# Kernel optimization log

Hardware: AMD Instinct MI355X
Metric: run time of the kernel (lower is better)

The kernel has to match this reference:

```python
import jax, jax.numpy as jnp
import numpy as np
from jax import lax

NUM_KEYPOINTS = 17
OUT_CHANNELS = 18
IN_CHANNELS = 480
H, W = 256, 256
MAX_PROPOSALS = 30
KPT_THRE = 0.01
CENTER_POOL_K = 3
# map_size = (H + W)/2 = 256; 200 < 256 <= 300 -> 5x5 max pool branch (static)
NMS_POOL_K = 5


def _avg_pool_same(x, k):
    # torch F.avg_pool2d(k, stride=1, pad=(k-1)//2), count_include_pad=True
    s = lax.reduce_window(x, 0.0, lax.add, (1, k, k), (1, 1, 1), 'SAME')
    return s / float(k * k)


def _max_pool_same(x, k):
    return lax.reduce_window(x, -jnp.inf, lax.max, (1, k, k), (1, 1, 1), 'SAME')


def setup_inputs() -> dict:
    key = jax.random.key(0)
    k1, k2 = jax.random.split(key)
    features = jax.random.normal(k1, (1, IN_CHANNELS, H, W), dtype=jnp.float32)
    conv_w = jax.random.normal(k2, (OUT_CHANNELS, IN_CHANNELS), dtype=jnp.float32) * 0.001
    # bias = -log((1-p)/p), p = 0.01
    conv_b = jnp.full((OUT_CHANNELS,), -np.log((1 - 0.01) / 0.01), dtype=jnp.float32)
    return {"features": features, "conv_w": conv_w, "conv_b": conv_b}


def reference(features, conv_w, conv_b):
    # 1x1 conv == channel contraction
    hm = jnp.einsum('bchw,oc->bohw', features, conv_w) + conv_b[None, :, None, None]
    hm = jnp.clip(jax.nn.sigmoid(hm), 1e-4, 1.0 - 1e-4)  # _sigmoid

    center = hm[:, -1, :, :]                 # [1, H, W] (no flip test)
    pool = _avg_pool_same(center, CENTER_POOL_K)
    center = (center + pool) * 0.5

    maxm = _max_pool_same(center, NMS_POOL_K)
    center = center * (maxm == center).astype(center.dtype)

    scores, pos_ind = lax.top_k(center.reshape(-1), MAX_PROPOSALS)
    x = pos_ind % W
    y = pos_ind // W
    instance_coord = jnp.stack((y, x), axis=1)            # [K, 2]
    # _sample_feats: features[0][:, y, x] -> [K, C]
    instance_param = features[0, :, y, x].T
    valid = scores > KPT_THRE                              # padded-select mask
    return instance_coord, scores, instance_param, valid
```

## Files before the change

### kernel.cpp

```cpp
#include <hip/hip_runtime.h>
#include <cfloat>
#include <cmath>

#define IC 480
#define OC 18
#define HH 256
#define WW 256
#define HW_ 65536
#define NPROP 30
#define CG 8
#define CPG 60
#define CAP 6144


__global__ __launch_bounds__(256) void k_dot(const float* __restrict__ f,
                                             const float* __restrict__ w,
                                             float* __restrict__ partial,
                                             int* __restrict__ counter) {
    __shared__ float sw[CPG];
    const int tid = threadIdx.x;
    const int cg = blockIdx.y;
    const int c0 = cg * CPG;
    if (tid < CPG) sw[tid] = w[17 * IC + c0 + tid];
    if (blockIdx.x == 0 && cg == 0 && tid == 0) *counter = 0;
    __syncthreads();
    const int p4 = blockIdx.x * 256 + tid;
    const float4* __restrict__ f4 = (const float4*)f;
    float ax = 0.f, ay = 0.f, az = 0.f, aw = 0.f;
    #pragma unroll 10
    for (int c = 0; c < CPG; ++c) {
        float4 v = f4[(size_t)(c0 + c) * (HW_ / 4) + p4];
        float wc = sw[c];
        ax = fmaf(v.x, wc, ax);
        ay = fmaf(v.y, wc, ay);
        az = fmaf(v.z, wc, az);
        aw = fmaf(v.w, wc, aw);
    }
    float4 r; r.x = ax; r.y = ay; r.z = az; r.w = aw;
    ((float4*)partial)[(size_t)cg * (HW_ / 4) + p4] = r;
}

__global__ __launch_bounds__(256) void k_pool(const float* __restrict__ partial,
                                              const float* __restrict__ conv_b,
                                              float* __restrict__ cand_val,
                                              int* __restrict__ cand_idx,
                                              int* __restrict__ counter) {
    const int TX = 32, TY = 8;
    __shared__ float sc[TY + 6][TX + 6];
    __shared__ float s2[TY + 4][TX + 4];
    const int tid = threadIdx.x;
    const int ox = blockIdx.x * TX, oy = blockIdx.y * TY;
    const float b = conv_b[OC - 1];

    for (int i = tid; i < (TY + 6) * (TX + 6); i += 256) {
        int ly = i / (TX + 6), lx = i % (TX + 6);
        int gy = oy - 3 + ly, gx = ox - 3 + lx;
        float v = 0.f;
        if (gy >= 0 && gy < HH && gx >= 0 && gx < WW) {
            int p = gy * WW + gx;
            float raw = b;
            #pragma unroll
            for (int g = 0; g < CG; ++g) raw += partial[g * HW_ + p];
            float s = 1.f / (1.f + expf(-raw));
            v = fminf(fmaxf(s, 1e-4f), 1.f - 1e-4f);
        }
        sc[ly][lx] = v;
    }
    __syncthreads();

    for (int i = tid; i < (TY + 4) * (TX + 4); i += 256) {
        int ly = i / (TX + 4), lx = i % (TX + 4);
        int gy = oy - 2 + ly, gx = ox - 2 + lx;
        float v = -FLT_MAX;
        if (gy >= 0 && gy < HH && gx >= 0 && gx < WW) {
            float sum = 0.f;
            #pragma unroll
            for (int dy = 0; dy < 3; ++dy)
                #pragma unroll
                for (int dx = 0; dx < 3; ++dx)
                    sum += sc[ly + dy][lx + dx];
            v = (sc[ly + 1][lx + 1] + sum / 9.0f) * 0.5f;
        }
        s2[ly][lx] = v;
    }
    __syncthreads();

    const int tx = tid & 31, ty = tid >> 5;
    float c = s2[ty + 2][tx + 2];
    float m = -FLT_MAX;
    #pragma unroll
    for (int dy = 0; dy < 5; ++dy)
        #pragma unroll
        for (int dx = 0; dx < 5; ++dx)
            m = fmaxf(m, s2[ty + dy][tx + dx]);
    if (m == c) {
        int slot = atomicAdd(counter, 1);
        if (slot < CAP) {
            cand_val[slot] = c;
            cand_idx[slot] = (oy + ty) * WW + (ox + tx);
        }
    }
}

__device__ __forceinline__ unsigned long long bsort64(unsigned long long key,
                                                      int lane) {
    #pragma unroll
    for (int k = 2; k <= 64; k <<= 1) {
        #pragma unroll
        for (int j = k >> 1; j > 0; j >>= 1) {
            unsigned long long o = __shfl_xor(key, j);
            bool lower = (lane & j) == 0;
            bool asc   = (lane & k) == 0;
            unsigned long long mn = key < o ? key : o;
            unsigned long long mx = key < o ? o : key;
            key = (lower == asc) ? mn : mx;
        }
    }
    return key;
}

__device__ __forceinline__ unsigned long long bmerge64(unsigned long long key,
                                                       int lane) {
    #pragma unroll
    for (int j = 32; j > 0; j >>= 1) {
        unsigned long long o = __shfl_xor(key, j);
        bool lower = (lane & j) == 0;
        unsigned long long mn = key < o ? key : o;
        unsigned long long mx = key < o ? o : key;
        key = lower ? mn : mx;
    }
    return key;
}

__global__ __launch_bounds__(512) void k_select(const float* __restrict__ cand_val,
                                                const int* __restrict__ cand_idx,
                                                const int* __restrict__ counter,
                                                float* __restrict__ out,
                                                int* __restrict__ selpix) {
    __shared__ unsigned long long lk[512];
    const int tid = threadIdx.x;
    const int lane = tid & 63, wv = tid >> 6;
    int n = *counter; if (n > CAP) n = CAP;

    unsigned long long R = 0;
    for (int base = wv * 64; base < n; base += 512) {
        int j = base + lane;
        unsigned long long key = 0;
        if (j < n) {
            unsigned fb = __float_as_uint(cand_val[j]);
            key = ((unsigned long long)fb << 32)
                | (unsigned long long)(0xFFFFFFFFu - (unsigned)cand_idx[j]);
        }
        key = bsort64(key, lane);
        unsigned long long crev = __shfl_xor(key, 63);
        R = R > crev ? R : crev;
        R = bmerge64(R, lane);
    }
    lk[tid] = R;
    __syncthreads();

    if (wv == 0) {
        R = lk[lane];
        #pragma unroll
        for (int w = 1; w < 8; ++w) {
            unsigned long long c = lk[w * 64 + lane];
            unsigned long long crev = __shfl_xor(c, 63);
            R = R > crev ? R : crev;
            R = bmerge64(R, lane);
        }
        int r = 63 - lane;
        if (r < NPROP) {
            float s = 0.f; int p = 0;
            if (R != 0) {
                s = __uint_as_float((unsigned)(R >> 32));
                p = (int)(0xFFFFFFFFu - (unsigned)(R & 0xFFFFFFFFu));
            }
            out[2 * r]     = (float)(p >> 8);
            out[2 * r + 1] = (float)(p & 255);
            out[60 + r] = s;
            out[60 + NPROP + NPROP * IC + r] = (s > 0.01f) ? 1.f : 0.f;
            selpix[r] = p;
        }
    }
}

__global__ __launch_bounds__(256) void k_gather(const float* __restrict__ f,
                                                const int* __restrict__ selpix,
                                                float* __restrict__ out) {
    __shared__ int sp[NPROP];
    const int tid = threadIdx.x;
    if (tid < NPROP) sp[tid] = selpix[tid];
    __syncthreads();
    int idx = blockIdx.x * 256 + tid;
    if (idx < IC * NPROP) {
        int c = idx / NPROP, i = idx % NPROP;
        out[60 + NPROP + idx] = f[(size_t)c * HW_ + sp[i]];
    }
}

extern "C" void kernel_launch(void* const* d_in, const int* in_sizes, int n_in,
                              void* d_out, int out_size, void* d_ws, size_t ws_size,
                              hipStream_t stream) {
    const float* features = (const float*)d_in[0];
    const float* conv_w   = (const float*)d_in[1];
    const float* conv_b   = (const float*)d_in[2];
    float* out = (float*)d_out;
    char* ws = (char*)d_ws;

    float* partial  = (float*)ws;
    float* cand_val = (float*)(ws + (2 << 20));
    int*   cand_idx = (int*)  (ws + (2 << 20) + CAP * 4);
    int*   counter  = (int*)  (ws + (2 << 20) + CAP * 8);
    int*   selpix   = (int*)  (ws + (2 << 20) + CAP * 8 + 16);

    k_dot   <<<dim3(HW_ / 1024, CG), 256, 0, stream>>>(features, conv_w,
                                                       partial, counter);
    k_pool  <<<dim3(WW / 32, HH / 8), 256, 0, stream>>>(partial, conv_b,
                                                        cand_val, cand_idx, counter);
    k_select<<<1, 512, 0, stream>>>(cand_val, cand_idx, counter, out, selpix);
    k_gather<<<(IC * NPROP + 255) / 256, 256, 0, stream>>>(features, selpix, out);
}
```

Before: 54.82 us.

## Fuse four kernels into one cooperative kernel with grid-wide syncs

Replaces the four separate launches (partial dot, pool/NMS, top-k select, gather) with a single cooperative kernel of 512 blocks that separates the stages with grid.sync(). The aim is to remove the launch overhead and inter-kernel gaps that dominate a short pipeline. The select stage now runs in one 256-thread block (4 waves instead of 8), so that serial phase does more work per wave. Each grid barrier adds its own cost, and a cooperative launch requires every block to be resident at once.

```diff
diff --git a/kernel.cpp b/kernel.cpp
--- a/kernel.cpp
+++ b/kernel.cpp
@@ -1,6 +1,9 @@
 #include <hip/hip_runtime.h>
+#include <hip/hip_cooperative_groups.h>
 #include <cfloat>
 #include <cmath>
+
+namespace cg = cooperative_groups;
 
 #define IC 480
 #define OC 18
@@ -8,99 +11,10 @@
 #define WW 256
 #define HW_ 65536
 #define NPROP 30
-#define CG 8
+#define NCG 8
 #define CPG 60
 #define CAP 6144
 
-
-__global__ __launch_bounds__(256) void k_dot(const float* __restrict__ f,
-                                             const float* __restrict__ w,
-                                             float* __restrict__ partial,
-                                             int* __restrict__ counter) {
-    __shared__ float sw[CPG];
-    const int tid = threadIdx.x;
-    const int cg = blockIdx.y;
-    const int c0 = cg * CPG;
-    if (tid < CPG) sw[tid] = w[17 * IC + c0 + tid];
-    if (blockIdx.x == 0 && cg == 0 && tid == 0) *counter = 0;
-    __syncthreads();
-    const int p4 = blockIdx.x * 256 + tid;
-    const float4* __restrict__ f4 = (const float4*)f;
-    float ax = 0.f, ay = 0.f, az = 0.f, aw = 0.f;
-    #pragma unroll 10
-    for (int c = 0; c < CPG; ++c) {
-        float4 v = f4[(size_t)(c0 + c) * (HW_ / 4) + p4];
-        float wc = sw[c];
-        ax = fmaf(v.x, wc, ax);
-        ay = fmaf(v.y, wc, ay);
-        az = fmaf(v.z, wc, az);
-        aw = fmaf(v.w, wc, aw);
-    }
-    float4 r; r.x = ax; r.y = ay; r.z = az; r.w = aw;
-    ((float4*)partial)[(size_t)cg * (HW_ / 4) + p4] = r;
-}
-
-__global__ __launch_bounds__(256) void k_pool(const float* __restrict__ partial,
-                                              const float* __restrict__ conv_b,
-                                              float* __restrict__ cand_val,
-                                              int* __restrict__ cand_idx,
-                                              int* __restrict__ counter) {
-    const int TX = 32, TY = 8;
-    __shared__ float sc[TY + 6][TX + 6];
-    __shared__ float s2[TY + 4][TX + 4];
-    const int tid = threadIdx.x;
-    const int ox = blockIdx.x * TX, oy = blockIdx.y * TY;
-    const float b = conv_b[OC - 1];
-
-    for (int i = tid; i < (TY + 6) * (TX + 6); i += 256) {
-        int ly = i / (TX + 6), lx = i % (TX + 6);
-        int gy = oy - 3 + ly, gx = ox - 3 + lx;
-        float v = 0.f;
-        if (gy >= 0 && gy < HH && gx >= 0 && gx < WW) {
-            int p = gy * WW + gx;
-            float raw = b;
-            #pragma unroll
-            for (int g = 0; g < CG; ++g) raw += partial[g * HW_ + p];
-            float s = 1.f / (1.f + expf(-raw));
-            v = fminf(fmaxf(s, 1e-4f), 1.f - 1e-4f);
-        }
-        sc[ly][lx] = v;
-    }
-    __syncthreads();
-
-    for (int i = tid; i < (TY + 4) * (TX + 4); i += 256) {
-        int ly = i / (TX + 4), lx = i % (TX + 4);
-        int gy = oy - 2 + ly, gx = ox - 2 + lx;
-        float v = -FLT_MAX;
-        if (gy >= 0 && gy < HH && gx >= 0 && gx < WW) {
-            float sum = 0.f;
-            #pragma unroll
-            for (int dy = 0; dy < 3; ++dy)
-                #pragma unroll
-                for (int dx = 0; dx < 3; ++dx)
-                    sum += sc[ly + dy][lx + dx];
-            v = (sc[ly + 1][lx + 1] + sum / 9.0f) * 0.5f;
-        }
-        s2[ly][lx] = v;
-    }
-    __syncthreads();
-
-    const int tx = tid & 31, ty = tid >> 5;
-    float c = s2[ty + 2][tx + 2];
-    float m = -FLT_MAX;
-    #pragma unroll
-    for (int dy = 0; dy < 5; ++dy)
-        #pragma unroll
-        for (int dx = 0; dx < 5; ++dx)
-            m = fmaxf(m, s2[ty + dy][tx + dx]);
-    if (m == c) {
-        int slot = atomicAdd(counter, 1);
-        if (slot < CAP) {
-            cand_val[slot] = c;
-            cand_idx[slot] = (oy + ty) * WW + (ox + tx);
-        }
-    }
-}
 
 __device__ __forceinline__ unsigned long long bsort64(unsigned long long key,
                                                       int lane) {
@@ -132,69 +46,152 @@
     return key;
 }
 
-__global__ __launch_bounds__(512) void k_select(const float* __restrict__ cand_val,
-                                                const int* __restrict__ cand_idx,
-                                                const int* __restrict__ counter,
-                                                float* __restrict__ out,
-                                                int* __restrict__ selpix) {
-    __shared__ unsigned long long lk[512];
+__global__ __launch_bounds__(256) void k_fused(const float* __restrict__ f,
+                                               const float* __restrict__ w,
+                                               const float* __restrict__ conv_b,
+                                               float* __restrict__ out,
+                                               float* __restrict__ partial,
+                                               float* __restrict__ cand_val,
+                                               int* __restrict__ cand_idx,
+                                               int* __restrict__ counter,
+                                               int* __restrict__ selpix) {
+    cg::grid_group grid = cg::this_grid();
     const int tid = threadIdx.x;
-    const int lane = tid & 63, wv = tid >> 6;
-    int n = *counter; if (n > CAP) n = CAP;
-
-    unsigned long long R = 0;
-    for (int base = wv * 64; base < n; base += 512) {
-        int j = base + lane;
-        unsigned long long key = 0;
-        if (j < n) {
-            unsigned fb = __float_as_uint(cand_val[j]);
-            key = ((unsigned long long)fb << 32)
-                | (unsigned long long)(0xFFFFFFFFu - (unsigned)cand_idx[j]);
-        }
-        key = bsort64(key, lane);
-        unsigned long long crev = __shfl_xor(key, 63);
-        R = R > crev ? R : crev;
-        R = bmerge64(R, lane);
-    }
-    lk[tid] = R;
-    __syncthreads();
-
-    if (wv == 0) {
-        R = lk[lane];
+    const int bid = blockIdx.x;
+
+    __shared__ float sw[CPG];
+    __shared__ float sc[14][38];
+    __shared__ float s2[12][36];
+    __shared__ unsigned long long lk[256];
+
+    {
+        const int cgi = bid >> 6;
+        const int bx  = bid & 63;
+        const int c0  = cgi * CPG;
+        if (tid < CPG) sw[tid] = w[17 * IC + c0 + tid];
+        if (bid == 0 && tid == 0) atomicExch(counter, 0);
+        __syncthreads();
+        const int p4 = bx * 256 + tid;
+        const float4* __restrict__ f4 = (const float4*)f;
+        float ax = 0.f, ay = 0.f, az = 0.f, aww = 0.f;
+        #pragma unroll 10
+        for (int c = 0; c < CPG; ++c) {
+            float4 v = f4[(size_t)(c0 + c) * (HW_ / 4) + p4];
+            float wc = sw[c];
+            ax  = fmaf(v.x, wc, ax);
+            ay  = fmaf(v.y, wc, ay);
+            az  = fmaf(v.z, wc, az);
+            aww = fmaf(v.w, wc, aww);
+        }
+        float4 r; r.x = ax; r.y = ay; r.z = az; r.w = aww;
+        ((float4*)partial)[(size_t)cgi * (HW_ / 4) + p4] = r;
+    }
+    grid.sync();
+
+    if (bid < 256) {
+        const int ox = (bid & 7) * 32, oy = (bid >> 3) * 8;
+        const float b = conv_b[OC - 1];
+        for (int i = tid; i < 14 * 38; i += 256) {
+            int ly = i / 38, lx = i % 38;
+            int gy = oy - 3 + ly, gx = ox - 3 + lx;
+            float v = 0.f;
+            if (gy >= 0 && gy < HH && gx >= 0 && gx < WW) {
+                int p = gy * WW + gx;
+                float raw = b;
+                #pragma unroll
+                for (int g = 0; g < NCG; ++g) raw += partial[g * HW_ + p];
+                float s = 1.f / (1.f + expf(-raw));
+                v = fminf(fmaxf(s, 1e-4f), 1.f - 1e-4f);
+            }
+            sc[ly][lx] = v;
+        }
+        __syncthreads();
+        for (int i = tid; i < 12 * 36; i += 256) {
+            int ly = i / 36, lx = i % 36;
+            int gy = oy - 2 + ly, gx = ox - 2 + lx;
+            float v = -FLT_MAX;
+            if (gy >= 0 && gy < HH && gx >= 0 && gx < WW) {
+                float sum = 0.f;
+                #pragma unroll
+                for (int dy = 0; dy < 3; ++dy)
+                    #pragma unroll
+                    for (int dx = 0; dx < 3; ++dx)
+                        sum += sc[ly + dy][lx + dx];
+                v = (sc[ly + 1][lx + 1] + sum / 9.0f) * 0.5f;
+            }
+            s2[ly][lx] = v;
+        }
+        __syncthreads();
+        const int tx = tid & 31, ty = tid >> 5;
+        float c = s2[ty + 2][tx + 2];
+        float m = -FLT_MAX;
         #pragma unroll
-        for (int w = 1; w < 8; ++w) {
-            unsigned long long c = lk[w * 64 + lane];
-            unsigned long long crev = __shfl_xor(c, 63);
+        for (int dy = 0; dy < 5; ++dy)
+            #pragma unroll
+            for (int dx = 0; dx < 5; ++dx)
+                m = fmaxf(m, s2[ty + dy][tx + dx]);
+        if (m == c) {
+            int slot = atomicAdd(counter, 1);
+            if (slot < CAP) {
+                cand_val[slot] = c;
+                cand_idx[slot] = (oy + ty) * WW + (ox + tx);
+            }
+        }
+    }
+    grid.sync();
+
+    if (bid == 0) {
+        const int lane = tid & 63, wv = tid >> 6;
+        int n = atomicAdd(counter, 0);
+        if (n > CAP) n = CAP;
+        unsigned long long R = 0;
+        for (int base = wv * 64; base < n; base += 256) {
+            int j = base + lane;
+            unsigned long long key = 0;
+            if (j < n) {
+                unsigned fb = __float_as_uint(cand_val[j]);
+                key = ((unsigned long long)fb << 32)
+                    | (unsigned long long)(0xFFFFFFFFu - (unsigned)cand_idx[j]);
+            }
+            key = bsort64(key, lane);
+            unsigned long long crev = __shfl_xor(key, 63);
             R = R > crev ? R : crev;
             R = bmerge64(R, lane);
         }
-        int r = 63 - lane;
-        if (r < NPROP) {
-            float s = 0.f; int p = 0;
-            if (R != 0) {
-                s = __uint_as_float((unsigned)(R >> 32));
-                p = (int)(0xFFFFFFFFu - (unsigned)(R & 0xFFFFFFFFu));
-            }
-            out[2 * r]     = (float)(p >> 8);
-            out[2 * r + 1] = (float)(p & 255);
-            out[60 + r] = s;
-            out[60 + NPROP + NPROP * IC + r] = (s > 0.01f) ? 1.f : 0.f;
-            selpix[r] = p;
-        }
-    }
-}
-
-__global__ __launch_bounds__(256) void k_gather(const float* __restrict__ f,
-                                                const int* __restrict__ selpix,
-                                                float* __restrict__ out) {
-    __shared__ int sp[NPROP];
-    const int tid = threadIdx.x;
-    if (tid < NPROP) sp[tid] = selpix[tid];
-    __syncthreads();
-    int idx = blockIdx.x * 256 + tid;
-    if (idx < IC * NPROP) {
-        int c = idx / NPROP, i = idx % NPROP;
-        out[60 + NPROP + idx] = f[(size_t)c * HW_ + sp[i]];
+        lk[tid] = R;
+        __syncthreads();
+        if (wv == 0) {
+            R = lk[lane];
+            #pragma unroll
+            for (int ww = 1; ww < 4; ++ww) {
+                unsigned long long c2 = lk[ww * 64 + lane];
+                unsigned long long crev = __shfl_xor(c2, 63);
+                R = R > crev ? R : crev;
+                R = bmerge64(R, lane);
+            }
+            int r = 63 - lane;
+            if (r < NPROP) {
+                float s = 0.f; int p = 0;
+                if (R != 0) {
+                    s = __uint_as_float((unsigned)(R >> 32));
+                    p = (int)(0xFFFFFFFFu - (unsigned)(R & 0xFFFFFFFFu));
+                }
+                out[2 * r]     = (float)(p >> 8);
+                out[2 * r + 1] = (float)(p & 255);
+                out[60 + r] = s;
+                out[60 + NPROP + NPROP * IC + r] = (s > 0.01f) ? 1.f : 0.f;
+                selpix[r] = p;
+            }
+        }
+    }
+    grid.sync();
+
+    {
+        int idx = bid * 256 + tid;
+        if (idx < IC * NPROP) {
+            int c = idx / NPROP, i = idx % NPROP;
+            out[60 + NPROP + idx] = f[(size_t)c * HW_ + selpix[i]];
+        }
     }
 }
 
@@ -213,10 +210,11 @@
     int*   counter  = (int*)  (ws + (2 << 20) + CAP * 8);
     int*   selpix   = (int*)  (ws + (2 << 20) + CAP * 8 + 16);
 
-    k_dot   <<<dim3(HW_ / 1024, CG), 256, 0, stream>>>(features, conv_w,
-                                                       partial, counter);
-    k_pool  <<<dim3(WW / 32, HH / 8), 256, 0, stream>>>(partial, conv_b,
-                                                        cand_val, cand_idx, counter);
-    k_select<<<1, 512, 0, stream>>>(cand_val, cand_idx, counter, out, selpix);
-    k_gather<<<(IC * NPROP + 255) / 256, 256, 0, stream>>>(features, selpix, out);
-}
+    void* args[9] = {
+        (void*)&features, (void*)&conv_w, (void*)&conv_b, (void*)&out,
+        (void*)&partial, (void*)&cand_val, (void*)&cand_idx,
+        (void*)&counter, (void*)&selpix
+    };
+    hipLaunchCooperativeKernel((const void*)k_fused, dim3(512), dim3(256),
+                               args, 0, stream);
+}
```

New measurement: 206.9 us. +277.5%, slower.

## Fuse pooling/NMS and top-k selection via last-block-done pattern

Applied to the files above, without the earlier changes.

Merges the pooling/NMS kernel and the single-block selection kernel into one launch. Each block increments a global done counter after emitting candidates, and the last block to finish performs the bitonic top-k over all candidates with 256 threads instead of 512. This removes one kernel launch and its inter-kernel gap, at the cost of a serialized tail in one block with fewer threads and extra atomics.

```diff
diff --git a/kernel.cpp b/kernel.cpp
--- a/kernel.cpp
+++ b/kernel.cpp
@@ -8,7 +8,7 @@
 #define WW 256
 #define HW_ 65536
 #define NPROP 30
-#define CG 8
+#define NCG 8
 #define CPG 60
 #define CAP 6144
 
@@ -16,13 +16,14 @@
 __global__ __launch_bounds__(256) void k_dot(const float* __restrict__ f,
                                              const float* __restrict__ w,
                                              float* __restrict__ partial,
-                                             int* __restrict__ counter) {
+                                             int* __restrict__ counter,
+                                             int* __restrict__ done) {
     __shared__ float sw[CPG];
     const int tid = threadIdx.x;
     const int cg = blockIdx.y;
     const int c0 = cg * CPG;
     if (tid < CPG) sw[tid] = w[17 * IC + c0 + tid];
-    if (blockIdx.x == 0 && cg == 0 && tid == 0) *counter = 0;
+    if (blockIdx.x == 0 && cg == 0 && tid == 0) { *counter = 0; *done = 0; }
     __syncthreads();
     const int p4 = blockIdx.x * 256 + tid;
     const float4* __restrict__ f4 = (const float4*)f;
@@ -38,68 +39,6 @@
     }
     float4 r; r.x = ax; r.y = ay; r.z = az; r.w = aw;
     ((float4*)partial)[(size_t)cg * (HW_ / 4) + p4] = r;
-}
-
-__global__ __launch_bounds__(256) void k_pool(const float* __restrict__ partial,
-                                              const float* __restrict__ conv_b,
-                                              float* __restrict__ cand_val,
-                                              int* __restrict__ cand_idx,
-                                              int* __restrict__ counter) {
-    const int TX = 32, TY = 8;
-    __shared__ float sc[TY + 6][TX + 6];
-    __shared__ float s2[TY + 4][TX + 4];
-    const int tid = threadIdx.x;
-    const int ox = blockIdx.x * TX, oy = blockIdx.y * TY;
-    const float b = conv_b[OC - 1];
-
-    for (int i = tid; i < (TY + 6) * (TX + 6); i += 256) {
-        int ly = i / (TX + 6), lx = i % (TX + 6);
-        int gy = oy - 3 + ly, gx = ox - 3 + lx;
-        float v = 0.f;
-        if (gy >= 0 && gy < HH && gx >= 0 && gx < WW) {
-            int p = gy * WW + gx;
-            float raw = b;
-            #pragma unroll
-            for (int g = 0; g < CG; ++g) raw += partial[g * HW_ + p];
-            float s = 1.f / (1.f + expf(-raw));
-            v = fminf(fmaxf(s, 1e-4f), 1.f - 1e-4f);
-        }
-        sc[ly][lx] = v;
-    }
-    __syncthreads();
-
-    for (int i = tid; i < (TY + 4) * (TX + 4); i += 256) {
-        int ly = i / (TX + 4), lx = i % (TX + 4);
-        int gy = oy - 2 + ly, gx = ox - 2 + lx;
-        float v = -FLT_MAX;
-        if (gy >= 0 && gy < HH && gx >= 0 && gx < WW) {
-            float sum = 0.f;
-            #pragma unroll
-            for (int dy = 0; dy < 3; ++dy)
-                #pragma unroll
-                for (int dx = 0; dx < 3; ++dx)
-                    sum += sc[ly + dy][lx + dx];
-            v = (sc[ly + 1][lx + 1] + sum / 9.0f) * 0.5f;
-        }
-        s2[ly][lx] = v;
-    }
-    __syncthreads();
-
-    const int tx = tid & 31, ty = tid >> 5;
-    float c = s2[ty + 2][tx + 2];
-    float m = -FLT_MAX;
-    #pragma unroll
-    for (int dy = 0; dy < 5; ++dy)
-        #pragma unroll
-        for (int dx = 0; dx < 5; ++dx)
-            m = fmaxf(m, s2[ty + dy][tx + dx]);
-    if (m == c) {
-        int slot = atomicAdd(counter, 1);
-        if (slot < CAP) {
-            cand_val[slot] = c;
-            cand_idx[slot] = (oy + ty) * WW + (ox + tx);
-        }
-    }
 }
 
 __device__ __forceinline__ unsigned long long bsort64(unsigned long long key,
@@ -132,24 +71,97 @@
     return key;
 }
 
-__global__ __launch_bounds__(512) void k_select(const float* __restrict__ cand_val,
-                                                const int* __restrict__ cand_idx,
-                                                const int* __restrict__ counter,
-                                                float* __restrict__ out,
-                                                int* __restrict__ selpix) {
-    __shared__ unsigned long long lk[512];
+__global__ __launch_bounds__(256) void k_pool_select(
+        const float* __restrict__ partial, const float* __restrict__ conv_b,
+        float* __restrict__ cand_val, int* __restrict__ cand_idx,
+        int* __restrict__ counter, int* __restrict__ done,
+        float* __restrict__ out, int* __restrict__ selpix) {
+    __shared__ float sc[14][38];
+    __shared__ float s2[12][36];
+    __shared__ unsigned long long lk[256];
+    __shared__ int isLast;
     const int tid = threadIdx.x;
+    const int ox = (blockIdx.x & 7) * 32, oy = (blockIdx.x >> 3) * 8;
+    const float b = conv_b[OC - 1];
+
+    for (int i = tid; i < 14 * 38; i += 256) {
+        int ly = i / 38, lx = i % 38;
+        int gy = oy - 3 + ly, gx = ox - 3 + lx;
+        float v = 0.f;
+        if (gy >= 0 && gy < HH && gx >= 0 && gx < WW) {
+            int p = gy * WW + gx;
+            float raw = b;
+            #pragma unroll
+            for (int g = 0; g < NCG; ++g) raw += partial[g * HW_ + p];
+            float s = 1.f / (1.f + expf(-raw));
+            v = fminf(fmaxf(s, 1e-4f), 1.f - 1e-4f);
+        }
+        sc[ly][lx] = v;
+    }
+    __syncthreads();
+
+    for (int i = tid; i < 12 * 36; i += 256) {
+        int ly = i / 36, lx = i % 36;
+        int gy = oy - 2 + ly, gx = ox - 2 + lx;
+        float v = -FLT_MAX;
+        if (gy >= 0 && gy < HH && gx >= 0 && gx < WW) {
+            float sum = 0.f;
+            #pragma unroll
+            for (int dy = 0; dy < 3; ++dy)
+                #pragma unroll
+                for (int dx = 0; dx < 3; ++dx)
+                    sum += sc[ly + dy][lx + dx];
+            v = (sc[ly + 1][lx + 1] + sum / 9.0f) * 0.5f;
+        }
+        s2[ly][lx] = v;
+    }
+    __syncthreads();
+
+    {
+        const int tx = tid & 31, ty = tid >> 5;
+        float c = s2[ty + 2][tx + 2];
+        float m = -FLT_MAX;
+        #pragma unroll
+        for (int dy = 0; dy < 5; ++dy)
+            #pragma unroll
+            for (int dx = 0; dx < 5; ++dx)
+                m = fmaxf(m, s2[ty + dy][tx + dx]);
+        if (m == c) {
+            int slot = atomicAdd(counter, 1);
+            if (slot < CAP) {
+                __hip_atomic_store(&cand_val[slot], c, __ATOMIC_RELAXED,
+                                   __HIP_MEMORY_SCOPE_AGENT);
+                __hip_atomic_store(&cand_idx[slot],
+                                   (oy + ty) * WW + (ox + tx),
+                                   __ATOMIC_RELAXED, __HIP_MEMORY_SCOPE_AGENT);
+            }
+        }
+    }
+    __syncthreads();
+    if (tid == 0) {
+        int prev = __hip_atomic_fetch_add(done, 1, __ATOMIC_ACQ_REL,
+                                          __HIP_MEMORY_SCOPE_AGENT);
+        isLast = (prev == 255);
+    }
+    __syncthreads();
+    if (!isLast) return;
+
     const int lane = tid & 63, wv = tid >> 6;
-    int n = *counter; if (n > CAP) n = CAP;
-
+    int n = __hip_atomic_load(counter, __ATOMIC_RELAXED,
+                              __HIP_MEMORY_SCOPE_AGENT);
+    if (n > CAP) n = CAP;
     unsigned long long R = 0;
-    for (int base = wv * 64; base < n; base += 512) {
+    for (int base = wv * 64; base < n; base += 256) {
         int j = base + lane;
         unsigned long long key = 0;
         if (j < n) {
-            unsigned fb = __float_as_uint(cand_val[j]);
+            float cv = __hip_atomic_load(&cand_val[j], __ATOMIC_RELAXED,
+                                         __HIP_MEMORY_SCOPE_AGENT);
+            int   ci = __hip_atomic_load(&cand_idx[j], __ATOMIC_RELAXED,
+                                         __HIP_MEMORY_SCOPE_AGENT);
+            unsigned fb = __float_as_uint(cv);
             key = ((unsigned long long)fb << 32)
-                | (unsigned long long)(0xFFFFFFFFu - (unsigned)cand_idx[j]);
+                | (unsigned long long)(0xFFFFFFFFu - (unsigned)ci);
         }
         key = bsort64(key, lane);
         unsigned long long crev = __shfl_xor(key, 63);
@@ -158,13 +170,12 @@
     }
     lk[tid] = R;
     __syncthreads();
-
     if (wv == 0) {
         R = lk[lane];
         #pragma unroll
-        for (int w = 1; w < 8; ++w) {
-            unsigned long long c = lk[w * 64 + lane];
-            unsigned long long crev = __shfl_xor(c, 63);
+        for (int ww = 1; ww < 4; ++ww) {
+            unsigned long long c2 = lk[ww * 64 + lane];
+            unsigned long long crev = __shfl_xor(c2, 63);
             R = R > crev ? R : crev;
             R = bmerge64(R, lane);
         }
@@ -211,12 +222,12 @@
     float* cand_val = (float*)(ws + (2 << 20));
     int*   cand_idx = (int*)  (ws + (2 << 20) + CAP * 4);
     int*   counter  = (int*)  (ws + (2 << 20) + CAP * 8);
+    int*   done     = (int*)  (ws + (2 << 20) + CAP * 8 + 8);
     int*   selpix   = (int*)  (ws + (2 << 20) + CAP * 8 + 16);
 
-    k_dot   <<<dim3(HW_ / 1024, CG), 256, 0, stream>>>(features, conv_w,
-                                                       partial, counter);
-    k_pool  <<<dim3(WW / 32, HH / 8), 256, 0, stream>>>(partial, conv_b,
-                                                        cand_val, cand_idx, counter);
-    k_select<<<1, 512, 0, stream>>>(cand_val, cand_idx, counter, out, selpix);
-    k_gather<<<(IC * NPROP + 255) / 256, 256, 0, stream>>>(features, selpix, out);
-}
+    k_dot        <<<dim3(HW_ / 1024, NCG), 256, 0, stream>>>(features, conv_w,
+                                                             partial, counter, done);
+    k_pool_select<<<256, 256, 0, stream>>>(partial, conv_b, cand_val, cand_idx,
+                                           counter, done, out, selpix);
+    k_gather     <<<(IC * NPROP + 255) / 256, 256, 0, stream>>>(features, selpix, out);
+}
```

Result: slower. 63.84 us (+16.5%).
